# Kernel tuning notes

Hardware: AMD Instinct MI355X
Metric: run time of the kernel (lower is better)

Reference implementation:

```python
import jax, jax.numpy as jnp
import numpy as np

EMB = 128
EA = 32
ET = 32
NN = 50000
NE = 320000
NBAND = 3
LAM = 0.01  # softshrink sparsity_threshold
LN_EPS = 1e-5


def _softshrink(x, lam=LAM):
    return jnp.where(x > lam, x - lam, jnp.where(x < -lam, x + lam, jnp.zeros_like(x)))


def _forward(hidden, edge_attr, edge_time_emb, boundary_condition,
             alpha, r1, i1, rb1, ib1, fre_w, fre_b,
             comb_w, comb_b, lin_w, lin_b, ln_g, ln_b, edge_index):
    num_nodes = hidden.shape[0]
    # gather source node features and concat edge features -> [E, d_in]
    x = jnp.concatenate([hidden[edge_index[0]], edge_attr, edge_time_emb], axis=1)
    # FreMLP: FFT over feature dim (real input -> complex64)
    x_fft = jnp.fft.fft(x)
    xr, xi = x_fft.real, x_fft.imag
    energy = jnp.sum(xr * xr + xi * xi, axis=-1)  # [E]
    energy_sum = jnp.sum(energy)
    outs = []
    for k in range(NBAND):
        factor = (2.0 * (k + 1) - 1.0) / (2.0 * NBAND)
        Qk = alpha[k] * factor * energy_sum
        bk = energy_sum / (alpha[k] * (2.0 * NBAND))
        mask = ((energy >= Qk - bk) & (energy <= Qk + bk)).astype(x.dtype)[:, None]
        fr = xr * mask
        fi = xi * mask
        # complex linear: (fr + i*fi) @ (r1 + i*i1) + (rb1 + i*ib1)
        o_r = fr @ r1[k] - fi @ i1[k] + rb1[k]
        o_i = fi @ r1[k] + fr @ i1[k] + ib1[k]
        o_r = _softshrink(jax.nn.relu(o_r))
        o_i = _softshrink(jax.nn.relu(o_i))
        outs.append(jax.lax.complex(o_r, o_i))
    y_fft = jnp.concatenate(outs, axis=-1)  # [E, NBAND*EMB] complex
    y = jnp.fft.ifft(y_fft).real
    msg = y @ fre_w + fre_b  # [E, EMB]
    # view_as_complex(msg, 0) -> view_as_real -> flatten: interleave real with zeros
    msg_ri = jnp.stack([msg, jnp.zeros_like(msg)], axis=-1).reshape(msg.shape[0], 2 * EMB)
    msg2 = msg_ri @ comb_w + comb_b  # [E, EMB]
    # scatter-reduce(sum) into destination nodes + boundary self-loops
    msg_aug = jnp.concatenate([msg2, boundary_condition], axis=0)
    idx_aug = jnp.concatenate([edge_index[1], jnp.arange(num_nodes, dtype=edge_index.dtype)])
    out = jax.ops.segment_sum(msg_aug, idx_aug, num_segments=num_nodes)
    out = out @ lin_w + lin_b
    mu = jnp.mean(out, axis=-1, keepdims=True)
    var = jnp.mean((out - mu) ** 2, axis=-1, keepdims=True)
    out = (out - mu) * jax.lax.rsqrt(var + LN_EPS) * ln_g + ln_b
    return jax.nn.relu(out)  # dropout is identity in eval mode


def setup_inputs() -> dict:
    key = jax.random.key(0)
    ks = jax.random.split(key, 16)
    d_in = EMB + EA + ET
    s = 0.02
    return {
        "hidden": jax.random.normal(ks[0], (NN, EMB), jnp.float32),
        "edge_attr": jax.random.normal(ks[1], (NE, EA), jnp.float32),
        "edge_time_emb": jax.random.normal(ks[2], (NE, ET), jnp.float32),
        "boundary_condition": jax.random.normal(ks[3], (NN, EMB), jnp.float32),
        "alpha": jnp.ones((NBAND,), jnp.float32),
        "r1": s * jax.random.normal(ks[4], (NBAND, d_in, EMB), jnp.float32),
        "i1": s * jax.random.normal(ks[5], (NBAND, d_in, EMB), jnp.float32),
        "rb1": s * jax.random.normal(ks[6], (NBAND, EMB), jnp.float32),
        "ib1": s * jax.random.normal(ks[7], (NBAND, EMB), jnp.float32),
        "fre_w": s * jax.random.normal(ks[8], (NBAND * EMB, EMB), jnp.float32),
        "fre_b": s * jax.random.normal(ks[9], (EMB,), jnp.float32),
        "comb_w": s * jax.random.normal(ks[10], (2 * EMB, EMB), jnp.float32),
        "comb_b": s * jax.random.normal(ks[11], (EMB,), jnp.float32),
        "lin_w": s * jax.random.normal(ks[12], (EMB, EMB), jnp.float32),
        "lin_b": s * jax.random.normal(ks[13], (EMB,), jnp.float32),
        "ln_g": jnp.ones((EMB,), jnp.float32),
        "ln_b": jnp.zeros((EMB,), jnp.float32),
        "edge_index": jax.random.randint(ks[14], (2, NE), 0, NN, dtype=jnp.int32),
    }


def reference(hidden, edge_attr, edge_time_emb, boundary_condition, alpha, r1, i1, rb1, ib1,
              fre_w, fre_b, comb_w, comb_b, lin_w, lin_b, ln_g, ln_b, edge_index):
    return _forward(hidden, edge_attr, edge_time_emb, boundary_condition, alpha, r1, i1,
                    rb1, ib1, fre_w, fre_b, comb_w, comb_b, lin_w, lin_b, ln_g, ln_b, edge_index)
```

## Files before the change

kernel.cpp:

```cpp
#include <hip/hip_runtime.h>
#include <hip/hip_bf16.h>

#define NNODES 50000
#define NEDGES 320000
#define EMB 128
#define DIN 192
#define NB 3
#define LAM 0.01f
#define LN_EPS 1e-5f
#define PI_F 3.14159265358979323846f

#define SCAN_B 196
#define SCAN_N (SCAN_B * 256)

#define TILES (NEDGES / 64)
#define EGRID 500
#define EITER (TILES / EGRID)

typedef __attribute__((ext_vector_type(8))) short v8s;
typedef __attribute__((ext_vector_type(4))) float v4f;
typedef __attribute__((ext_vector_type(2))) float v2f;
typedef __attribute__((ext_vector_type(2))) unsigned v2u;

#define WS_ESUM 0
#define WS_WB   16
#define WS_G2B  (WS_WB + 73728)
#define WS_G2   (WS_G2B + 49152)
#define WS_PHI  (WS_G2 + 98304)
#define WS_M    (WS_PHI + 98304)
#define WS_BB   (WS_M + 16384)
#define WS_GB2  (WS_BB + 768)
#define WS_CK   (WS_GB2 + 128)
#define WS_EN   (WS_CK + 384)
#define WS_NORM (WS_EN + NEDGES)
#define WS_CNT  (WS_NORM + NNODES)
#define WS_CUR  (WS_CNT + SCAN_N)
#define WS_PART (WS_CUR + SCAN_N)
#define WS_EIDS (WS_PART + 256)
#define WS_LWB  (WS_EIDS + NEDGES)

__device__ __forceinline__ unsigned pk2(float a, float b) {
  __hip_bfloat162 h2 = __float22bfloat162_rn(make_float2(a, b));
  return *reinterpret_cast<unsigned*>(&h2);
}

__device__ __forceinline__ void atomic2(float* dp, float a, float b) {
#if __has_builtin(__builtin_amdgcn_flat_atomic_fadd_v2f32)
  v2f val; val.x = a; val.y = b;
  __builtin_amdgcn_flat_atomic_fadd_v2f32((v2f*)dp, val);
#else
  atomicAdd(dp, a); atomicAdd(dp + 1, b);
#endif
}

__device__ __forceinline__ void bar_lds() {
  asm volatile("s_waitcnt lgkmcnt(0)" ::: "memory");
  __builtin_amdgcn_s_barrier();
  asm volatile("" ::: "memory");
}

__global__ __launch_bounds__(256) void k_prep1(
    const float* __restrict__ r1, const float* __restrict__ i1,
    __hip_bfloat16* __restrict__ Wb, const float* __restrict__ comb_w,
    const float* __restrict__ lin_w, float* __restrict__ M,
    const float* __restrict__ fre_w, float* __restrict__ Phi,
    const float* __restrict__ hidden, float* __restrict__ norms,
    float* __restrict__ outz, int* __restrict__ cnt, float* __restrict__ esum,
    __hip_bfloat16* __restrict__ lwb) {
  __shared__ float cs[384], sn[384];
  const int t = threadIdx.x;
  const int b = blockIdx.x;
  if (b < 576) {
    if (t < 192) sincosf((2.f * PI_F / 192.f) * (float)t, &sn[t], &cs[t]);
    __syncthreads();
    int idx = b * 256 + t;
    int n = idx / 768, c = idx - (idx / 768) * 768;
    int k = c >> 8, col = c & 255;
    int isI = col >> 7, j = col & 127;
    const float* ap = (isI ? i1 : r1) + (size_t)k * DIN * EMB + j;
    const float* bp = (isI ? r1 : i1) + (size_t)k * DIN * EMB + j;
    float sgn = isI ? -1.f : 1.f;
    float acc = 0.f;
    int m = 0;
    for (int f = 0; f < DIN; ++f) {
      acc = fmaf(cs[m], ap[(size_t)f * EMB], fmaf(sgn * sn[m], bp[(size_t)f * EMB], acc));
      m += n; if (m >= 192) m -= 192;
    }
    int kc = n >> 5, quad = (n & 31) >> 3, jj = n & 7;
    int lane = quad * 16 + (col & 15);
    Wb[((((k * 6 + kc) * 16 + (col >> 4)) * 64) + lane) * 8 + jj] = __float2bfloat16(acc);
  } else if (b < 640) {
    int idx = (b - 576) * 256 + t;
    int j = idx >> 7, j2 = idx & 127;
    float acc = 0.f;
    for (int tt = 0; tt < 128; ++tt)
      acc = fmaf(comb_w[(2 * j) * 128 + tt], lin_w[tt * 128 + j2], acc);
    M[idx] = acc;
  } else if (b < 704) {
    int idx = (b - 640) * 256 + t;
    int kk = idx >> 7, col = idx & 127;
    int kc = kk >> 5, quad2 = (kk & 31) >> 3, jj = kk & 7;
    lwb[(((kc * 8 + (col >> 4)) * 64) + quad2 * 16 + (col & 15)) * 8 + jj] =
        __float2bfloat16(lin_w[kk * 128 + col]);
  } else if (b < 1088) {
    for (int i = t; i < 384; i += 256)
      sincosf((2.f * PI_F / 384.f) * (float)i, &sn[i], &cs[i]);
    __syncthreads();
    int idx = (b - 704) * 256 + t;
    int slot = idx >> 7, j1 = idx & 127;
    int k = slot >> 8, r = slot & 255;
    int isI = r >> 7;
    int f = k * 128 + (r & 127);
    const float* tp = isI ? sn : cs;
    float sg = isI ? -1.f : 1.f;
    float acc = 0.f;
    int m = 0;
    for (int n = 0; n < 384; ++n) {
      acc = fmaf(sg * tp[m], fre_w[n * 128 + j1], acc);
      m += f; if (m >= 384) m -= 384;
    }
    Phi[slot * 128 + j1] = acc * (1.f / 384.f);
  } else if (b < 13588) {
    const int w = t >> 6, lane = t & 63;
    const int n = (b - 1088) * 4 + w;
    const float2 v = ((const float2*)(hidden + (size_t)n * 128))[lane];
    float ss = v.x * v.x + v.y * v.y;
#pragma unroll
    for (int off = 32; off > 0; off >>= 1) ss += __shfl_xor(ss, off, 64);
    if (lane == 0) norms[n] = ss;
    float2 z; z.x = 0.f; z.y = 0.f;
    ((float2*)(outz + (size_t)n * 128))[lane] = z;
  } else if (b < 13784) {
    cnt[(b - 13588) * 256 + t] = 0;
  } else {
    if (t < 16) esum[t] = 0.f;
  }
}

__global__ __launch_bounds__(256) void k_prep2(
    const float* __restrict__ Phi, const float* __restrict__ M,
    float* __restrict__ G2, __hip_bfloat16* __restrict__ G2b,
    const float* __restrict__ norms, const float* __restrict__ eattr,
    const float* __restrict__ ett, const int* __restrict__ eidx,
    float* __restrict__ energies, float* __restrict__ esum,
    int* __restrict__ cnt) {
  const int t = threadIdx.x;
  const int b = blockIdx.x;
  if (b < 384) {
    int idx = b * 256 + t;
    int slot = idx >> 7, j2 = idx & 127;
    float acc = 0.f;
    for (int j1 = 0; j1 < 128; ++j1)
      acc = fmaf(Phi[slot * 128 + j1], M[j1 * 128 + j2], acc);
    G2[idx] = acc;
    int k = slot >> 8, s = slot & 255;
    int kc = s >> 5, quad = (s & 31) >> 3, jj = s & 7;
    G2b[((((k * 8 + kc) * 8 + (j2 >> 4)) * 64) + quad * 16 + (j2 & 15)) * 8 + jj] =
        __float2bfloat16(acc);
  } else {
    int e = (b - 384) * 256 + t;
    float ss = norms[eidx[e]];
    const float4* a4 = (const float4*)(eattr + (size_t)e * 32);
#pragma unroll
    for (int i = 0; i < 8; ++i) {
      float4 v = a4[i];
      ss += v.x * v.x + v.y * v.y + v.z * v.z + v.w * v.w;
    }
    const float4* t4 = (const float4*)(ett + (size_t)e * 32);
#pragma unroll
    for (int i = 0; i < 8; ++i) {
      float4 v = t4[i];
      ss += v.x * v.x + v.y * v.y + v.z * v.z + v.w * v.w;
    }
    float en = 192.f * ss;
    energies[e] = en;
    float tot = en;
#pragma unroll
    for (int off = 32; off > 0; off >>= 1) tot += __shfl_down(tot, off, 64);
    if ((t & 63) == 0) atomicAdd(esum, tot);
    atomicAdd(&cnt[eidx[NEDGES + e]], 1);
  }
}

__global__ __launch_bounds__(256) void k_prep3(
    const float* __restrict__ rb1, const float* __restrict__ ib1,
    const float* __restrict__ fre_b, const float* __restrict__ comb_b,
    const float* __restrict__ lin_w, const float* __restrict__ M,
    const float* __restrict__ G2, float* __restrict__ bb,
    float* __restrict__ gb2, float* __restrict__ ck,
    int* __restrict__ cnt, int* __restrict__ part) {
  __shared__ int sm[256];
  const int t = threadIdx.x;
  const int b = blockIdx.x;
  if (b < 5) {
    int idx = b * 256 + t;
    if (idx < 768) {
      int k = idx >> 8, r = idx & 255;
      bb[idx] = (r >= 128) ? ib1[k * 128 + (r & 127)] : rb1[k * 128 + r];
    } else if (idx < 896) {
      int j2 = idx - 768;
      float acc = 0.f;
      for (int j = 0; j < 128; ++j) acc += fre_b[j] * M[j * 128 + j2];
      for (int tt = 0; tt < 128; ++tt) acc += comb_b[tt] * lin_w[tt * 128 + j2];
      gb2[j2] = acc;
    } else if (idx < 1280) {
      int q = idx - 896;
      int k = q >> 7, j2 = q & 127;
      float acc = 0.f;
      for (int j = 0; j < 128; ++j) {
        float vr = rb1[k * 128 + j];
        vr = fmaxf(vr, 0.f); vr = (vr > LAM) ? vr - LAM : 0.f;
        float vi = ib1[k * 128 + j];
        vi = fmaxf(vi, 0.f); vi = (vi > LAM) ? vi - LAM : 0.f;
        acc += vr * G2[(k * 256 + j) * 128 + j2] + vi * G2[(k * 256 + 128 + j) * 128 + j2];
      }
      ck[k * 128 + j2] = acc;
    }
  } else {
    int blk = b - 5;
    int i = blk * 256 + t;
    int v = (i < NNODES) ? cnt[i] : 0;
    sm[t] = v;
    __syncthreads();
#pragma unroll
    for (int off = 1; off < 256; off <<= 1) {
      int x = (t >= off) ? sm[t - off] : 0;
      __syncthreads();
      sm[t] += x;
      __syncthreads();
    }
    cnt[i] = sm[t] - v;
    if (t == 255) part[blk] = sm[t];
  }
}

__global__ __launch_bounds__(256) void k_scan(const int* __restrict__ cnt,
                                              const int* __restrict__ part,
                                              int* __restrict__ cur) {
  __shared__ int sm[256];
  const int t = threadIdx.x;
  const int b = blockIdx.x;
  sm[t] = (t < b) ? part[t] : 0;
  __syncthreads();
#pragma unroll
  for (int off = 128; off > 0; off >>= 1) {
    if (t < off) sm[t] += sm[t + off];
    __syncthreads();
  }
  cur[b * 256 + t] = cnt[b * 256 + t] + sm[0];
}

__global__ __launch_bounds__(256) void k_fill(const int* __restrict__ eidx,
                                              int* __restrict__ cur,
                                              int* __restrict__ eids) {
  int e = blockIdx.x * 256 + threadIdx.x;
  int pos = atomicAdd(&cur[eidx[NEDGES + e]], 1);
  eids[pos] = e;
}

#define XS_STR 200
#define OS_STR 264
#define ZS_STR 132

#define LOADM_PUBLISH(B)                                                       \
  do {                                                                         \
    if (t < 3) tileact[B][t] = 0;                                              \
    if (t < 64) {                                                              \
      eid_s[B][t] = eidA;                                                      \
      srcs[B][t] = srcA;                                                       \
      dsts[B][t] = dstA;                                                       \
      _Pragma("unroll") for (int k = 0; k < NB; ++k) {                         \
        bool m_ = (enA >= lo[k]) && (enA <= hi[k]);                            \
        maskf[B][k][t] = m_ ? 1.f : 0.f;                                       \
        if (m_) atomicOr(&tileact[B][k], 1);                                   \
      }                                                                        \
    }                                                                          \
  } while (0)

#define GATHER(B)                                                              \
  do {                                                                         \
    const int eh = t >> 5, ch = (t & 31) * 4;                                  \
    hr0 = *(const float4*)(hidden + (size_t)srcs[B][eh] * 128 + ch);           \
    hr1 = *(const float4*)(hidden + (size_t)srcs[B][eh + 16] * 128 + ch);      \
    hr2 = *(const float4*)(hidden + (size_t)srcs[B][eh + 32] * 128 + ch);      \
    hr3 = *(const float4*)(hidden + (size_t)srcs[B][eh + 48] * 128 + ch);      \
    const int ea = t >> 4, q = t & 15;                                         \
    const float* p0 = (q < 8) ? eattr + (size_t)eid_s[B][ea] * 32 + q * 4      \
                              : ett + (size_t)eid_s[B][ea] * 32 + (q - 8) * 4; \
    ar0 = *(const float4*)p0;                                                  \
    const float* p1 = (q < 8) ? eattr + (size_t)eid_s[B][ea + 32] * 32 + q * 4 \
                              : ett + (size_t)eid_s[B][ea + 32] * 32 + (q - 8) * 4; \
    ar1 = *(const float4*)p1;                                                  \
  } while (0)

#define WRITEX()                                                               \
  do {                                                                         \
    const int eh = t >> 5, ch = (t & 31) * 4;                                  \
    v2u u;                                                                     \
    u.x = pk2(hr0.x, hr0.y); u.y = pk2(hr0.z, hr0.w);                          \
    *(v2u*)&Xs[eh * XS_STR + ch] = u;                                          \
    u.x = pk2(hr1.x, hr1.y); u.y = pk2(hr1.z, hr1.w);                          \
    *(v2u*)&Xs[(eh + 16) * XS_STR + ch] = u;                                   \
    u.x = pk2(hr2.x, hr2.y); u.y = pk2(hr2.z, hr2.w);                          \
    *(v2u*)&Xs[(eh + 32) * XS_STR + ch] = u;                                   \
    u.x = pk2(hr3.x, hr3.y); u.y = pk2(hr3.z, hr3.w);                          \
    *(v2u*)&Xs[(eh + 48) * XS_STR + ch] = u;                                   \
    const int ea = t >> 4, q4 = (t & 15) * 4;                                  \
    u.x = pk2(ar0.x, ar0.y); u.y = pk2(ar0.z, ar0.w);                          \
    *(v2u*)&Xs[ea * XS_STR + 128 + q4] = u;                                    \
    u.x = pk2(ar1.x, ar1.y); u.y = pk2(ar1.z, ar1.w);                          \
    *(v2u*)&Xs[(ea + 32) * XS_STR + 128 + q4] = u;                             \
  } while (0)

__global__ __launch_bounds__(512, 2) void k_edges(
    const float* __restrict__ hidden, const float* __restrict__ eattr,
    const float* __restrict__ ett, const float* __restrict__ alpha,
    const int* __restrict__ eidx, const int* __restrict__ eids,
    const __hip_bfloat16* __restrict__ Wb, const __hip_bfloat16* __restrict__ G2b,
    const float* __restrict__ bb, const float* __restrict__ gb2,
    const float* __restrict__ ck, const float* __restrict__ energies,
    const float* __restrict__ esum, float* __restrict__ accum) {
  __shared__ __align__(16) char smem[64 * XS_STR * 2 + 64 * OS_STR * 2];
  short* Xs = (short*)smem;
  short* Os = (short*)(smem + 64 * XS_STR * 2);
  float* Zs = (float*)smem;
  __shared__ float maskf[2][3][64];
  __shared__ int eid_s[2][64], srcs[2][64], dsts[2][64];
  __shared__ int tileact[2][3];

  const int t = threadIdx.x;
  const int lane = t & 63, w = t >> 6;
  const int quad = lane >> 4, lc = lane & 15;
  const int we = w >> 2, wc = w & 3;
  const int tile = blockIdx.x;

  float lo[NB], hi[NB];
  {
    const float es = *esum;
#pragma unroll
    for (int k = 0; k < NB; ++k) {
      float a = alpha[k];
      float factor = (2.f * (k + 1) - 1.f) / (2.f * NB);
      float Q = a * factor * es;
      float bw = es / (a * (2.f * NB));
      lo[k] = Q - bw;
      hi[k] = Q + bw;
    }
  }

  float4 hr0, hr1, hr2, hr3, ar0, ar1;
  int eidA = 0, srcA = 0, dstA = 0, eidB = 0;
  float enA = 0.f;

  if (t < 64) {
    int e_ = eids[tile * 64 + t];
    eidA = e_; srcA = eidx[e_]; dstA = eidx[NEDGES + e_]; enA = energies[e_];
  }
  LOADM_PUBLISH(0);
  if (t < 64) {
    int e_ = eids[(tile + EGRID) * 64 + t];
    eidA = e_; srcA = eidx[e_]; dstA = eidx[NEDGES + e_]; enA = energies[e_];
    eidB = eids[(tile + 2 * EGRID) * 64 + t];
  }
  bar_lds();
  GATHER(0);

#pragma unroll 1
  for (int ti = 0; ti < EITER; ++ti) {
    const int cb = ti & 1;
    WRITEX();
    if (ti + 1 < EITER) LOADM_PUBLISH(cb ^ 1);
    if (t < 64) {
      if (ti + 2 < EITER) {
        eidA = eidB;
        srcA = eidx[eidB]; dstA = eidx[NEDGES + eidB]; enA = energies[eidB];
      }
      if (ti + 3 < EITER)
        eidB = eids[(tile + (ti + 3) * EGRID) * 64 + t];
    }
    bar_lds();

    v4f acc2[2][2];
#pragma unroll
    for (int m2 = 0; m2 < 2; ++m2)
#pragma unroll
      for (int ct = 0; ct < 2; ++ct)
#pragma unroll
        for (int r = 0; r < 4; ++r) acc2[m2][ct][r] = 0.f;

    for (int k = 0; k < NB; ++k) {
      if (!tileact[cb][k]) continue;
      v4f accA[4][2];
#pragma unroll
      for (int mt = 0; mt < 4; ++mt)
#pragma unroll
        for (int n = 0; n < 2; ++n)
#pragma unroll
          for (int r = 0; r < 4; ++r) accA[mt][n][r] = 0.f;

#pragma unroll
      for (int kc = 0; kc < 6; ++kc) {
        v8s af[4];
#pragma unroll
        for (int mt = 0; mt < 4; ++mt)
          af[mt] = *(const v8s*)&Xs[(mt * 16 + lc) * XS_STR + kc * 32 + quad * 8];
        const __hip_bfloat16* wp = Wb + ((((k * 6 + kc) * 16 + 2 * w) * 64) + lane) * 8;
#pragma unroll
        for (int ntl = 0; ntl < 2; ++ntl) {
          v8s bfr = *(const v8s*)(const void*)(wp + ntl * 512);
#pragma unroll
          for (int mt = 0; mt < 4; ++mt)
            accA[mt][ntl] =
                __builtin_amdgcn_mfma_f32_16x16x32_bf16(bfr, af[mt], accA[mt][ntl], 0, 0, 0);
        }
      }
      bar_lds();
#pragma unroll
      for (int mt = 0; mt < 4; ++mt) {
        const float mk = maskf[cb][k][mt * 16 + lc];
#pragma unroll
        for (int ntl = 0; ntl < 2; ++ntl) {
          const int colb = w * 32 + ntl * 16 + quad * 4;
          const float4 bbv = *(const float4*)&bb[k * 256 + colb];
          float v0 = fmaf(mk, accA[mt][ntl][0], bbv.x);
          float v1 = fmaf(mk, accA[mt][ntl][1], bbv.y);
          float v2 = fmaf(mk, accA[mt][ntl][2], bbv.z);
          float v3 = fmaf(mk, accA[mt][ntl][3], bbv.w);
          v0 = fmaxf(v0, 0.f); v0 = (v0 > LAM) ? v0 - LAM : 0.f;
          v1 = fmaxf(v1, 0.f); v1 = (v1 > LAM) ? v1 - LAM : 0.f;
          v2 = fmaxf(v2, 0.f); v2 = (v2 > LAM) ? v2 - LAM : 0.f;
          v3 = fmaxf(v3, 0.f); v3 = (v3 > LAM) ? v3 - LAM : 0.f;
          v2u u; u.x = pk2(v0, v1); u.y = pk2(v2, v3);
          *(v2u*)&Os[(mt * 16 + lc) * OS_STR + colb] = u;
        }
      }
      bar_lds();
#pragma unroll
      for (int kc = 0; kc < 8; ++kc) {
        v8s of0 = *(const v8s*)&Os[(we * 32 + lc) * OS_STR + kc * 32 + quad * 8];
        v8s of1 = *(const v8s*)&Os[(we * 32 + 16 + lc) * OS_STR + kc * 32 + quad * 8];
#pragma unroll
        for (int ct = 0; ct < 2; ++ct) {
          v8s g = *(const v8s*)(const void*)(
              G2b + ((((k * 8 + kc) * 8 + (wc * 2 + ct)) * 64) + lane) * 8);
          acc2[0][ct] = __builtin_amdgcn_mfma_f32_16x16x32_bf16(g, of0, acc2[0][ct], 0, 0, 0);
          acc2[1][ct] = __builtin_amdgcn_mfma_f32_16x16x32_bf16(g, of1, acc2[1][ct], 0, 0, 0);
        }
      }
    }

    if (ti + 1 < EITER) GATHER(cb ^ 1);

    bar_lds();
#pragma unroll
    for (int ct = 0; ct < 2; ++ct) {
      const int colb = wc * 32 + ct * 16 + quad * 4;
      float4 base = *(const float4*)&gb2[colb];
#pragma unroll
      for (int k = 0; k < NB; ++k)
        if (!tileact[cb][k]) {
          const float4 cv = *(const float4*)&ck[k * 128 + colb];
          base.x += cv.x; base.y += cv.y; base.z += cv.z; base.w += cv.w;
        }
#pragma unroll
      for (int m2 = 0; m2 < 2; ++m2) {
        const int rowz = we * 32 + m2 * 16 + lc;
        float4 zz;
        zz.x = acc2[m2][ct][0] + base.x;
        zz.y = acc2[m2][ct][1] + base.y;
        zz.z = acc2[m2][ct][2] + base.z;
        zz.w = acc2[m2][ct][3] + base.w;
        *(float4*)&Zs[rowz * ZS_STR + colb] = zz;
      }
    }
    bar_lds();
    if (w < 4) {
      int c = 2 * lane;
      int r0 = w * 16;
      float s0 = 0.f, s1 = 0.f;
#pragma unroll
      for (int r = 0; r < 16; ++r) {
        int row = r0 + r;
        const float2 z = *(const float2*)&Zs[row * ZS_STR + c];
        s0 += z.x; s1 += z.y;
        int d = dsts[cb][row];
        if (r == 15 || dsts[cb][row + 1] != d) {
          atomic2(accum + (size_t)d * 128 + c, s0, s1);
          s0 = 0.f; s1 = 0.f;
        }
      }
    }
    if (ti + 1 < EITER) bar_lds();
  }
}

__global__ __launch_bounds__(256) void k_nodes(
    const float* __restrict__ boundary, const __hip_bfloat16* __restrict__ lwb,
    const float* __restrict__ lin_b, const float* __restrict__ ln_g,
    const float* __restrict__ ln_b, float* __restrict__ out) {
  __shared__ __align__(16) short Bs[64 * 136];
  __shared__ __align__(16) float Zs[64 * 132];
  const int t = threadIdx.x;
  const int w = t >> 6, lane = t & 63;
  const int quad = lane >> 4, lc = lane & 15;
  const int n0 = blockIdx.x * 64;
#pragma unroll
  for (int it = 0; it < 8; ++it) {
    int fi = it * 256 + t;
    int row = fi >> 5, c4 = fi & 31;
    float4 v = make_float4(0.f, 0.f, 0.f, 0.f);
    if (n0 + row < NNODES)
      v = *(const float4*)(boundary + (size_t)(n0 + row) * 128 + c4 * 4);
    v2u u; u.x = pk2(v.x, v.y); u.y = pk2(v.z, v.w);
    *(v2u*)&Bs[row * 136 + c4 * 4] = u;
  }
  __syncthreads();
  const int we = w >> 1, wc = w & 1;
  v4f acc[2][4];
#pragma unroll
  for (int m2 = 0; m2 < 2; ++m2)
#pragma unroll
    for (int ct = 0; ct < 4; ++ct)
#pragma unroll
      for (int r = 0; r < 4; ++r) acc[m2][ct][r] = 0.f;
#pragma unroll
  for (int kc = 0; kc < 4; ++kc) {
    v8s b0 = *(const v8s*)&Bs[(we * 32 + lc) * 136 + kc * 32 + quad * 8];
    v8s b1 = *(const v8s*)&Bs[(we * 32 + 16 + lc) * 136 + kc * 32 + quad * 8];
#pragma unroll
    for (int ct = 0; ct < 4; ++ct) {
      v8s af = *(const v8s*)(const void*)(
          lwb + (((kc * 8 + (wc * 4 + ct)) * 64) + lane) * 8);
      acc[0][ct] = __builtin_amdgcn_mfma_f32_16x16x32_bf16(af, b0, acc[0][ct], 0, 0, 0);
      acc[1][ct] = __builtin_amdgcn_mfma_f32_16x16x32_bf16(af, b1, acc[1][ct], 0, 0, 0);
    }
  }
#pragma unroll
  for (int m2 = 0; m2 < 2; ++m2)
#pragma unroll
    for (int ct = 0; ct < 4; ++ct) {
      const int colb = wc * 64 + ct * 16 + quad * 4;
      const int row = we * 32 + m2 * 16 + lc;
      float4 z;
      z.x = acc[m2][ct][0]; z.y = acc[m2][ct][1];
      z.z = acc[m2][ct][2]; z.w = acc[m2][ct][3];
      *(float4*)&Zs[row * 132 + colb] = z;
    }
  __syncthreads();
  const int c = 2 * lane;
  const float2 lb = *(const float2*)&lin_b[c];
  const float2 gg = *(const float2*)&ln_g[c];
  const float2 bbv = *(const float2*)&ln_b[c];
#pragma unroll 1
  for (int i = 0; i < 16; ++i) {
    int row = w * 16 + i;
    int n = n0 + row;
    if (n >= NNODES) break;
    const float2 z = *(const float2*)&Zs[row * 132 + c];
    const float2 ob = *(const float2*)&out[(size_t)n * 128 + c];
    float a0 = z.x + ob.x + lb.x;
    float a1 = z.y + ob.y + lb.y;
    float s = a0 + a1, sq = a0 * a0 + a1 * a1;
#pragma unroll
    for (int off = 32; off > 0; off >>= 1) {
      s += __shfl_xor(s, off, 64);
      sq += __shfl_xor(sq, off, 64);
    }
    float mu = s * (1.f / 128.f);
    float var = sq * (1.f / 128.f) - mu * mu;
    float rs = 1.f / sqrtf(var + LN_EPS);
    float2 o;
    o.x = fmaxf((a0 - mu) * rs * gg.x + bbv.x, 0.f);
    o.y = fmaxf((a1 - mu) * rs * gg.y + bbv.y, 0.f);
    *(float2*)&out[(size_t)n * 128 + c] = o;
  }
}

extern "C" void kernel_launch(void* const* d_in, const int* in_sizes, int n_in,
                              void* d_out, int out_size, void* d_ws, size_t ws_size,
                              hipStream_t stream) {
  const float* hidden   = (const float*)d_in[0];
  const float* eattr    = (const float*)d_in[1];
  const float* ett      = (const float*)d_in[2];
  const float* boundary = (const float*)d_in[3];
  const float* alpha    = (const float*)d_in[4];
  const float* r1       = (const float*)d_in[5];
  const float* i1       = (const float*)d_in[6];
  const float* rb1      = (const float*)d_in[7];
  const float* ib1      = (const float*)d_in[8];
  const float* fre_w    = (const float*)d_in[9];
  const float* fre_b    = (const float*)d_in[10];
  const float* comb_w   = (const float*)d_in[11];
  const float* comb_b   = (const float*)d_in[12];
  const float* lin_w    = (const float*)d_in[13];
  const float* lin_b    = (const float*)d_in[14];
  const float* ln_g     = (const float*)d_in[15];
  const float* ln_b     = (const float*)d_in[16];
  const int*   eidx     = (const int*)d_in[17];
  float* ws  = (float*)d_ws;
  float* out = (float*)d_out;
  __hip_bfloat16* Wb  = (__hip_bfloat16*)(ws + WS_WB);
  __hip_bfloat16* G2b = (__hip_bfloat16*)(ws + WS_G2B);
  __hip_bfloat16* lwb = (__hip_bfloat16*)(ws + WS_LWB);
  int* cnt  = (int*)(ws + WS_CNT);
  int* cur  = (int*)(ws + WS_CUR);
  int* part = (int*)(ws + WS_PART);
  int* eids = (int*)(ws + WS_EIDS);

  k_prep1<<<13785, 256, 0, stream>>>(r1, i1, Wb, comb_w, lin_w, ws + WS_M,
                                     fre_w, ws + WS_PHI, hidden, ws + WS_NORM,
                                     out, cnt, ws + WS_ESUM, lwb);
  k_prep2<<<384 + NEDGES / 256, 256, 0, stream>>>(ws + WS_PHI, ws + WS_M, ws + WS_G2,
                                                  G2b, ws + WS_NORM, eattr, ett, eidx,
                                                  ws + WS_EN, ws + WS_ESUM, cnt);
  k_prep3<<<5 + SCAN_B, 256, 0, stream>>>(rb1, ib1, fre_b, comb_b, lin_w, ws + WS_M,
                                          ws + WS_G2, ws + WS_BB, ws + WS_GB2,
                                          ws + WS_CK, cnt, part);
  k_scan<<<SCAN_B, 256, 0, stream>>>(cnt, part, cur);
  k_fill<<<NEDGES / 256, 256, 0, stream>>>(eidx, cur, eids);
  k_edges<<<EGRID, 512, 0, stream>>>(hidden, eattr, ett, alpha, eidx, eids,
                                     Wb, G2b, ws + WS_BB, ws + WS_GB2,
                                     ws + WS_CK, ws + WS_EN, ws + WS_ESUM, out);
  k_nodes<<<(NNODES + 63) / 64, 256, 0, stream>>>(boundary, lwb, lin_b, ln_g, ln_b, out);
}
```

Measured before the change: 483.9 us.

## Remap second GEMM so each wave owns a 16-column slice; halve grid

The second MFMA stage now has each of the 8 waves compute all 64 rows for one 16-column slice, instead of a 32x32 block per wave. This loads one G2 fragment per k-chunk rather than two, while reading four O-row fragments from LDS instead of two. The persistent grid is also halved so each block loops over twice as many tiles, which amortises the setup and prefetch pipeline but lowers parallelism across CUs.

```diff
diff --git a/kernel.cpp b/kernel.cpp
--- a/kernel.cpp
+++ b/kernel.cpp
@@ -14,7 +14,7 @@
 #define SCAN_N (SCAN_B * 256)
 
 #define TILES (NEDGES / 64)
-#define EGRID 500
+#define EGRID 250
 #define EITER (TILES / EGRID)
 
 typedef __attribute__((ext_vector_type(8))) short v8s;
@@ -331,7 +331,6 @@
   const int t = threadIdx.x;
   const int lane = t & 63, w = t >> 6;
   const int quad = lane >> 4, lc = lane & 15;
-  const int we = w >> 2, wc = w & 3;
   const int tile = blockIdx.x;
 
   float lo[NB], hi[NB];
@@ -380,13 +379,11 @@
     }
     bar_lds();
 
-    v4f acc2[2][2];
-#pragma unroll
-    for (int m2 = 0; m2 < 2; ++m2)
-#pragma unroll
-      for (int ct = 0; ct < 2; ++ct)
-#pragma unroll
-        for (int r = 0; r < 4; ++r) acc2[m2][ct][r] = 0.f;
+    v4f acc2[4];
+#pragma unroll
+    for (int mt = 0; mt < 4; ++mt)
+#pragma unroll
+      for (int r = 0; r < 4; ++r) acc2[mt][r] = 0.f;
 
     for (int k = 0; k < NB; ++k) {
       if (!tileact[cb][k]) continue;
@@ -437,24 +434,23 @@
       bar_lds();
 #pragma unroll
       for (int kc = 0; kc < 8; ++kc) {
-        v8s of0 = *(const v8s*)&Os[(we * 32 + lc) * OS_STR + kc * 32 + quad * 8];
-        v8s of1 = *(const v8s*)&Os[(we * 32 + 16 + lc) * OS_STR + kc * 32 + quad * 8];
-#pragma unroll
-        for (int ct = 0; ct < 2; ++ct) {
-          v8s g = *(const v8s*)(const void*)(
-              G2b + ((((k * 8 + kc) * 8 + (wc * 2 + ct)) * 64) + lane) * 8);
-          acc2[0][ct] = __builtin_amdgcn_mfma_f32_16x16x32_bf16(g, of0, acc2[0][ct], 0, 0, 0);
-          acc2[1][ct] = __builtin_amdgcn_mfma_f32_16x16x32_bf16(g, of1, acc2[1][ct], 0, 0, 0);
-        }
+        v8s of[4];
+#pragma unroll
+        for (int mt = 0; mt < 4; ++mt)
+          of[mt] = *(const v8s*)&Os[(mt * 16 + lc) * OS_STR + kc * 32 + quad * 8];
+        v8s g = *(const v8s*)(const void*)(
+            G2b + ((((k * 8 + kc) * 8 + w) * 64) + lane) * 8);
+#pragma unroll
+        for (int mt = 0; mt < 4; ++mt)
+          acc2[mt] = __builtin_amdgcn_mfma_f32_16x16x32_bf16(g, of[mt], acc2[mt], 0, 0, 0);
       }
     }
 
     if (ti + 1 < EITER) GATHER(cb ^ 1);
 
     bar_lds();
-#pragma unroll
-    for (int ct = 0; ct < 2; ++ct) {
-      const int colb = wc * 32 + ct * 16 + quad * 4;
+    {
+      const int colb = w * 16 + quad * 4;
       float4 base = *(const float4*)&gb2[colb];
 #pragma unroll
       for (int k = 0; k < NB; ++k)
@@ -463,13 +459,13 @@
           base.x += cv.x; base.y += cv.y; base.z += cv.z; base.w += cv.w;
         }
 #pragma unroll
-      for (int m2 = 0; m2 < 2; ++m2) {
-        const int rowz = we * 32 + m2 * 16 + lc;
+      for (int mt = 0; mt < 4; ++mt) {
+        const int rowz = mt * 16 + lc;
         float4 zz;
-        zz.x = acc2[m2][ct][0] + base.x;
-        zz.y = acc2[m2][ct][1] + base.y;
-        zz.z = acc2[m2][ct][2] + base.z;
-        zz.w = acc2[m2][ct][3] + base.w;
+        zz.x = acc2[mt][0] + base.x;
+        zz.y = acc2[mt][1] + base.y;
+        zz.z = acc2[mt][2] + base.z;
+        zz.w = acc2[mt][3] + base.w;
         *(float4*)&Zs[rowz * ZS_STR + colb] = zz;
       }
     }
```

After: 459.9 us. -5.0%, faster.
